# Kernel optimization log

Measured on AMD Instinct MI355X. Metric: run time of the kernel, lower is better.

Reference implementation:

```python
import jax, jax.numpy as jnp
import numpy as np

B, N, D, L = 4, 256, 512, 3  # batch, seq_len, input_dim, n_layer


def setup_inputs() -> dict:
    key = jax.random.key(0)
    ks = jax.random.split(key, 12)
    s = 0.02
    return {
        "x": jax.random.normal(ks[0], (B, N, D), dtype=jnp.float32),
        # Highway: L layers, each a gate Linear(D,D) and transform Linear(D,D)
        "hw_gate_w": jax.random.normal(ks[1], (L, D, D), dtype=jnp.float32) * s,
        "hw_gate_b": jnp.zeros((L, D), dtype=jnp.float32),
        "hw_tr_w": jax.random.normal(ks[2], (L, D, D), dtype=jnp.float32) * s,
        "hw_tr_b": jnp.zeros((L, D), dtype=jnp.float32),
        # link_weight MLP: Linear(2D,D) -> ReLU -> [Linear(D,D) -> ReLU]*(L-2) -> Linear(D,1) -> Sigmoid
        "lw0_w": jax.random.normal(ks[3], (D, 2 * D), dtype=jnp.float32) * s,
        "lw0_b": jnp.zeros((D,), dtype=jnp.float32),
        "lw1_w": jax.random.normal(ks[4], (D, D), dtype=jnp.float32) * s,
        "lw1_b": jnp.zeros((D,), dtype=jnp.float32),
        "lwo_w": jax.random.normal(ks[5], (1, D), dtype=jnp.float32) * s,
        "lwo_b": jnp.zeros((1,), dtype=jnp.float32),
    }


def _highway(x, gw, gb, tw, tb):
    # standard highway: y = g * relu(Wt x + bt) + (1 - g) * x, g = sigmoid(Wg x + bg)
    for i in range(gw.shape[0]):
        g = jax.nn.sigmoid(jnp.einsum('bnd,ed->bne', x, gw[i]) + gb[i])
        t = jax.nn.relu(jnp.einsum('bnd,ed->bne', x, tw[i]) + tb[i])
        x = g * t + (1.0 - g) * x
    return x


def reference(x, hw_gate_w, hw_gate_b, hw_tr_w, hw_tr_b,
              lw0_w, lw0_b, lw1_w, lw1_b, lwo_w, lwo_b):
    d = x.shape[-1]
    h = _highway(x, hw_gate_w, hw_gate_b, hw_tr_w, hw_tr_b)  # [B,N,D]
    # Fused pairwise-concat + first Linear: cat(h_i, h_j) @ W0.T ==
    # h_i @ W0[:, :D].T + h_j @ W0[:, D:].T  (avoids the [B,N*N,2D] tensor)
    a = jnp.einsum('bnd,ed->bne', h, lw0_w[:, :d])  # uses m1 (row i)
    b = jnp.einsum('bnd,ed->bne', h, lw0_w[:, d:])  # uses m2 (col j)
    z = jax.nn.relu(a[:, :, None, :] + b[:, None, :, :] + lw0_b)  # [B,N,N,D]
    # (dropout is identity in eval mode)
    z = jax.nn.relu(jnp.einsum('bijd,ed->bije', z, lw1_w) + lw1_b)  # n_layer-2 == 1 hidden layer
    out = jax.nn.sigmoid(jnp.einsum('bijd,d->bij', z, lwo_w[0]) + lwo_b[0])
    return out  # [B,N,N]
```

## Files before the change

### kernel.cpp

```cpp
#include <hip/hip_runtime.h>
#include <hip/hip_bf16.h>

#define BB 4
#define NN 256
#define DD 512

using short8   = __attribute__((ext_vector_type(8))) short;
using f32x4    = __attribute__((ext_vector_type(4))) float;
using uint32x4 = __attribute__((ext_vector_type(4))) unsigned int;

__device__ __forceinline__ unsigned short f2bf(float f) {
    unsigned int u = __float_as_uint(f);
    unsigned int r = (u + 0x7fffu + ((u >> 16) & 1u)) >> 16;
    return (unsigned short)r;
}

__device__ __forceinline__ unsigned cvtpk(float lo, float hi) {
    unsigned r;
    asm("v_cvt_pk_bf16_f32 %0, %1, %2" : "=v"(r) : "v"(lo), "v"(hi));
    return r;
}

template <int ROWS, int NW>
__device__ __forceinline__ void stage_rows(const unsigned short* src, int stride,
                                           short* dst, int tid) {
    int wave = tid >> 6, lane = tid & 63;
#pragma unroll
    for (int c = 0; c < ROWS / (8 * NW); ++c) {
        int rbase = (c * NW + wave) * 8;
        int row   = rbase + (lane >> 3);
        int slot  = (lane & 7) ^ (row & 7);
        const unsigned short* g = src + (size_t)row * stride + slot * 8;
        __builtin_amdgcn_global_load_lds(
            (const __attribute__((address_space(1))) void*)g,
            (__attribute__((address_space(3))) void*)(dst + rbase * 64),
            16, 0, 0);
    }
}

__device__ __forceinline__ short8 read_frag(const short* T, int rowBase, int k2) {
    int lane = threadIdx.x & 63;
    int row  = rowBase + (lane & 15);
    int slot = ((k2 * 4) + (lane >> 4)) ^ (row & 7);
    return *(const short8*)(T + row * 64 + slot * 8);
}

__global__ void prep_kernel(const float* __restrict__ x,
                            const float* __restrict__ gw, const float* __restrict__ tw,
                            const float* __restrict__ w0, const float* __restrict__ w1,
                            float* __restrict__ h0_f32, unsigned short* __restrict__ h0_bf,
                            unsigned short* __restrict__ wg_bf, unsigned short* __restrict__ wt_bf,
                            unsigned short* __restrict__ w0c_bf, unsigned short* __restrict__ w1_bf) {
    const int S_X = BB * NN * DD;
    const int S_W = 3 * DD * DD;
    const int S_W0 = 2 * DD * DD;
    int total = S_X + S_W + S_W + S_W0 + DD * DD;
    for (int idx = blockIdx.x * blockDim.x + threadIdx.x; idx < total;
         idx += gridDim.x * blockDim.x) {
        int t = idx;
        if (t < S_X) { float v = x[t]; h0_f32[t] = v; h0_bf[t] = f2bf(v); continue; }
        t -= S_X;
        if (t < S_W) { wg_bf[t] = f2bf(gw[t]); continue; }
        t -= S_W;
        if (t < S_W) { wt_bf[t] = f2bf(tw[t]); continue; }
        t -= S_W;
        if (t < S_W0) {
            int e = t >> 9, d = t & 511;
            float v = (e < DD) ? w0[e * (2 * DD) + d] : w0[(e - DD) * (2 * DD) + DD + d];
            w0c_bf[t] = f2bf(v); continue;
        }
        t -= S_W0;
        w1_bf[t] = f2bf(w1[t]);
    }
}

__global__ __launch_bounds__(256) void highway_kernel(
        const float* __restrict__ h_in, const unsigned short* __restrict__ hbf_in,
        const unsigned short* __restrict__ wg_bf, const unsigned short* __restrict__ wt_bf,
        const float* __restrict__ gb, const float* __restrict__ tb,
        float* __restrict__ h_out, unsigned short* __restrict__ hbf_out) {
    __shared__ short ht[64 * 64];
    __shared__ short wgt[64 * 64];
    __shared__ short wtt[64 * 64];
    int tid = threadIdx.x, lane = tid & 63, wave = tid >> 6;
    int mt = blockIdx.x >> 3, et = blockIdx.x & 7;
    int m0 = mt * 64, e0 = et * 64;
    int wm = wave >> 1, we = wave & 1;
    f32x4 gacc[2][2] = {}, tacc[2][2] = {};
    for (int ks = 0; ks < 8; ++ks) {
        int d0 = ks * 64;
        __syncthreads();
        stage_rows<64, 4>(hbf_in + (size_t)m0 * DD + d0, DD, ht, tid);
        stage_rows<64, 4>(wg_bf + (size_t)e0 * DD + d0, DD, wgt, tid);
        stage_rows<64, 4>(wt_bf + (size_t)e0 * DD + d0, DD, wtt, tid);
        __syncthreads();
#pragma unroll
        for (int k2 = 0; k2 < 2; ++k2) {
            short8 af[2], bg[2], bt[2];
#pragma unroll
            for (int f = 0; f < 2; ++f) af[f] = read_frag(ht, wm * 32 + f * 16, k2);
#pragma unroll
            for (int f = 0; f < 2; ++f) bg[f] = read_frag(wgt, we * 32 + f * 16, k2);
#pragma unroll
            for (int f = 0; f < 2; ++f) bt[f] = read_frag(wtt, we * 32 + f * 16, k2);
#pragma unroll
            for (int fm = 0; fm < 2; ++fm)
#pragma unroll
                for (int fn = 0; fn < 2; ++fn) {
                    gacc[fm][fn] = __builtin_amdgcn_mfma_f32_16x16x32_bf16(af[fm], bg[fn], gacc[fm][fn], 0, 0, 0);
                    tacc[fm][fn] = __builtin_amdgcn_mfma_f32_16x16x32_bf16(af[fm], bt[fn], tacc[fm][fn], 0, 0, 0);
                }
        }
    }
#pragma unroll
    for (int fm = 0; fm < 2; ++fm)
#pragma unroll
        for (int fn = 0; fn < 2; ++fn) {
            int e = e0 + we * 32 + fn * 16 + (lane & 15);
            float gbe = gb[e], tbe = tb[e];
#pragma unroll
            for (int r = 0; r < 4; ++r) {
                int m = m0 + wm * 32 + fm * 16 + (lane >> 4) * 4 + r;
                float g = 1.f / (1.f + __expf(-(gacc[fm][fn][r] + gbe)));
                float tv = tacc[fm][fn][r] + tbe; tv = tv > 0.f ? tv : 0.f;
                float ho = h_in[(size_t)m * DD + e];
                float hn = g * tv + (1.f - g) * ho;
                h_out[(size_t)m * DD + e] = hn;
                hbf_out[(size_t)m * DD + e] = f2bf(hn);
            }
        }
}

__global__ __launch_bounds__(256) void ab_kernel(
        const unsigned short* __restrict__ hbf, const unsigned short* __restrict__ w0c_bf,
        const float* __restrict__ lw0_b,
        float* __restrict__ a_out, float* __restrict__ b_out) {
    __shared__ short ht[64 * 64];
    __shared__ short wt_[128 * 64];
    int tid = threadIdx.x, lane = tid & 63, wave = tid >> 6;
    int mt = blockIdx.x >> 3, et = blockIdx.x & 7;
    int m0 = mt * 64, e0 = et * 128;
    int wm = wave >> 1, we = wave & 1;
    f32x4 acc[2][4] = {};
    for (int ks = 0; ks < 8; ++ks) {
        __syncthreads();
        stage_rows<64, 4>(hbf + (size_t)m0 * DD + ks * 64, DD, ht, tid);
        stage_rows<128, 4>(w0c_bf + (size_t)e0 * DD + ks * 64, DD, wt_, tid);
        __syncthreads();
#pragma unroll
        for (int k2 = 0; k2 < 2; ++k2) {
            short8 af[2], bf_[4];
#pragma unroll
            for (int f = 0; f < 2; ++f) af[f] = read_frag(ht, wm * 32 + f * 16, k2);
#pragma unroll
            for (int f = 0; f < 4; ++f) bf_[f] = read_frag(wt_, we * 64 + f * 16, k2);
#pragma unroll
            for (int fm = 0; fm < 2; ++fm)
#pragma unroll
                for (int fn = 0; fn < 4; ++fn)
                    acc[fm][fn] = __builtin_amdgcn_mfma_f32_16x16x32_bf16(af[fm], bf_[fn], acc[fm][fn], 0, 0, 0);
        }
    }
#pragma unroll
    for (int fm = 0; fm < 2; ++fm)
#pragma unroll
        for (int fn = 0; fn < 4; ++fn) {
            int e = e0 + we * 64 + fn * 16 + (lane & 15);
#pragma unroll
            for (int r = 0; r < 4; ++r) {
                int m = m0 + wm * 32 + fm * 16 + (lane >> 4) * 4 + r;
                float v = acc[fm][fn][r];
                if (e < DD) a_out[(size_t)m * DD + e] = v + lw0_b[e];
                else        b_out[(size_t)m * DD + (e - DD)] = v;
            }
        }
}


#define Z_LOADS(K)                                                            \
    {                                                                         \
        const int dl_ = (K) * 64 + s * 8;                                     \
        alo = *(const f32x4*)(arow + dl_);                                    \
        ahi = *(const f32x4*)(arow + dl_ + 4);                                \
        const float* b0_ = brow + (size_t)rr * DD + dl_;                      \
        const float* b1_ = brow + (size_t)(64 + rr) * DD + dl_;               \
        b0lo = *(const f32x4*)b0_; b0hi = *(const f32x4*)(b0_ + 4);           \
        b1lo = *(const f32x4*)b1_; b1hi = *(const f32x4*)(b1_ + 4);           \
    }

#define Z_MATH()                                                              \
    {                                                                         \
        zw0[0] = cvtpk(fmaxf(alo[0] + b0lo[0], 0.f), fmaxf(alo[1] + b0lo[1], 0.f)); \
        zw0[1] = cvtpk(fmaxf(alo[2] + b0lo[2], 0.f), fmaxf(alo[3] + b0lo[3], 0.f)); \
        zw0[2] = cvtpk(fmaxf(ahi[0] + b0hi[0], 0.f), fmaxf(ahi[1] + b0hi[1], 0.f)); \
        zw0[3] = cvtpk(fmaxf(ahi[2] + b0hi[2], 0.f), fmaxf(ahi[3] + b0hi[3], 0.f)); \
        zw1[0] = cvtpk(fmaxf(alo[0] + b1lo[0], 0.f), fmaxf(alo[1] + b1lo[1], 0.f)); \
        zw1[1] = cvtpk(fmaxf(alo[2] + b1lo[2], 0.f), fmaxf(alo[3] + b1lo[3], 0.f)); \
        zw1[2] = cvtpk(fmaxf(ahi[0] + b1hi[0], 0.f), fmaxf(ahi[1] + b1hi[1], 0.f)); \
        zw1[3] = cvtpk(fmaxf(ahi[2] + b1hi[2], 0.f), fmaxf(ahi[3] + b1hi[3], 0.f)); \
    }

#define Z_WRITE(BUF)                                                          \
    {                                                                         \
        *(uint32x4*)((BUF) + rr * 64 + ((s ^ (rr & 7)) * 8)) = zw0;           \
        const int r1_ = 64 + rr;                                              \
        *(uint32x4*)((BUF) + r1_ * 64 + ((s ^ (r1_ & 7)) * 8)) = zw1;         \
    }

__global__ __launch_bounds__(512, 2) void pair_kernel(
        const float* __restrict__ a_f32, const float* __restrict__ b_f32,
        const unsigned short* __restrict__ w1_bf,
        const float* __restrict__ lw1_b, const float* __restrict__ lwo_w,
        const float* __restrict__ lwo_b, float* __restrict__ out) {
    __shared__ short ws[2][512 * 64];
    __shared__ short zs[2][128 * 64];
    int tid = threadIdx.x, lane = tid & 63, wave = tid >> 6;
    int bid = blockIdx.x;
    int swz = (bid & 7) * 256 + (bid >> 3);
    int bb = swz >> 9, i = (swz >> 1) & 255, j0 = (swz & 1) * 128;
    const float* arow = a_f32 + (size_t)(bb * NN + i) * DD;
    const float* brow = b_f32 + (size_t)(bb * NN + j0) * DD;
    int s = tid & 7, rr = tid >> 3;
    int we = wave;

    f32x4 acc[8][4] = {};
    uint32x4 zw0, zw1;
    f32x4 alo, ahi, b0lo, b0hi, b1lo, b1hi;

    Z_LOADS(0)
    __builtin_amdgcn_sched_barrier(0);
    stage_rows<512, 8>(w1_bf, DD, ws[0], tid);
    __builtin_amdgcn_sched_barrier(0);
    Z_MATH()
    Z_WRITE(zs[0])
    asm volatile("s_waitcnt lgkmcnt(0)" ::: "memory");
    __builtin_amdgcn_s_barrier();
    asm volatile("s_waitcnt vmcnt(0)" ::: "memory");
    __builtin_amdgcn_s_barrier();

#pragma unroll
    for (int k = 0; k < 8; ++k) {
        const short* zc = zs[k & 1];
        const short* wc = ws[k & 1];

        if (k < 7) {
            Z_LOADS(k + 1)
            __builtin_amdgcn_sched_barrier(0);
            stage_rows<512, 8>(w1_bf + (size_t)(k + 1) * 64, DD,
                               ws[(k + 1) & 1], tid);
            __builtin_amdgcn_sched_barrier(0);
        }

#pragma unroll
        for (int k2 = 0; k2 < 2; ++k2) {
            short8 bfr[4];
#pragma unroll
            for (int f = 0; f < 4; ++f) bfr[f] = read_frag(wc, we * 64 + f * 16, k2);
#pragma unroll
            for (int fh = 0; fh < 2; ++fh) {
                short8 af[4];
#pragma unroll
                for (int f = 0; f < 4; ++f) af[f] = read_frag(zc, (fh * 4 + f) * 16, k2);
                __builtin_amdgcn_s_setprio(1);
#pragma unroll
                for (int fm = 0; fm < 4; ++fm)
#pragma unroll
                    for (int fn = 0; fn < 4; ++fn)
                        acc[fh * 4 + fm][fn] = __builtin_amdgcn_mfma_f32_16x16x32_bf16(
                            af[fm], bfr[fn], acc[fh * 4 + fm][fn], 0, 0, 0);
                __builtin_amdgcn_s_setprio(0);
            }
        }

        if (k < 7) {
            Z_MATH()
            Z_WRITE(zs[(k + 1) & 1])
            asm volatile("s_waitcnt lgkmcnt(0)" ::: "memory");
        }
        __builtin_amdgcn_s_barrier();
        if (k < 7) {
            asm volatile("s_waitcnt vmcnt(0)" ::: "memory");
            __builtin_amdgcn_s_barrier();
        }
    }

    __syncthreads();
    float* s_red = (float*)zs;
#pragma unroll
    for (int fm = 0; fm < 8; ++fm) {
        float red[4] = {0.f, 0.f, 0.f, 0.f};
#pragma unroll
        for (int fn = 0; fn < 4; ++fn) {
            int e = we * 64 + fn * 16 + (lane & 15);
            float b1e = lw1_b[e], woe = lwo_w[e];
#pragma unroll
            for (int r = 0; r < 4; ++r) {
                float v = acc[fm][fn][r] + b1e;
                red[r] += (v > 0.f) ? v * woe : 0.f;
            }
        }
#pragma unroll
        for (int mask = 1; mask < 16; mask <<= 1)
#pragma unroll
            for (int r = 0; r < 4; ++r) red[r] += __shfl_xor(red[r], mask, 64);
        if ((lane & 15) == 0) {
#pragma unroll
            for (int r = 0; r < 4; ++r)
                s_red[we * 128 + fm * 16 + (lane >> 4) * 4 + r] = red[r];
        }
    }
    __syncthreads();
    if (tid < 128) {
        float v = lwo_b[0];
#pragma unroll
        for (int w8 = 0; w8 < 8; ++w8) v += s_red[w8 * 128 + tid];
        out[((size_t)(bb * NN + i)) * NN + j0 + tid] = 1.f / (1.f + __expf(-v));
    }
}

extern "C" void kernel_launch(void* const* d_in, const int* in_sizes, int n_in,
                              void* d_out, int out_size, void* d_ws, size_t ws_size,
                              hipStream_t stream) {
    const float* x    = (const float*)d_in[0];
    const float* gw   = (const float*)d_in[1];
    const float* gb   = (const float*)d_in[2];
    const float* tw   = (const float*)d_in[3];
    const float* tb   = (const float*)d_in[4];
    const float* w0   = (const float*)d_in[5];
    const float* w0b  = (const float*)d_in[6];
    const float* w1   = (const float*)d_in[7];
    const float* w1b_ = (const float*)d_in[8];
    const float* wo   = (const float*)d_in[9];
    const float* wob  = (const float*)d_in[10];
    float* out = (float*)d_out;

    char* w = (char*)d_ws;
    float* hA  = (float*)w;            w += (size_t)BB * NN * DD * 4;
    float* hB  = (float*)w;            w += (size_t)BB * NN * DD * 4;
    unsigned short* hbA = (unsigned short*)w; w += (size_t)BB * NN * DD * 2;
    unsigned short* hbB = (unsigned short*)w; w += (size_t)BB * NN * DD * 2;
    float* a_f = (float*)w;            w += (size_t)BB * NN * DD * 4;
    float* b_f = (float*)w;            w += (size_t)BB * NN * DD * 4;
    unsigned short* wg_bf  = (unsigned short*)w; w += (size_t)3 * DD * DD * 2;
    unsigned short* wt_bf  = (unsigned short*)w; w += (size_t)3 * DD * DD * 2;
    unsigned short* w0c_bf = (unsigned short*)w; w += (size_t)2 * DD * DD * 2;
    unsigned short* w1_bf  = (unsigned short*)w; w += (size_t)DD * DD * 2;

    prep_kernel<<<1024, 256, 0, stream>>>(x, gw, tw, w0, w1, hA, hbA, wg_bf, wt_bf, w0c_bf, w1_bf);

    highway_kernel<<<128, 256, 0, stream>>>(hA, hbA, wg_bf + 0 * DD * DD, wt_bf + 0 * DD * DD,
                                            gb + 0 * DD, tb + 0 * DD, hB, hbB);
    highway_kernel<<<128, 256, 0, stream>>>(hB, hbB, wg_bf + 1 * DD * DD, wt_bf + 1 * DD * DD,
                                            gb + 1 * DD, tb + 1 * DD, hA, hbA);
    highway_kernel<<<128, 256, 0, stream>>>(hA, hbA, wg_bf + 2 * DD * DD, wt_bf + 2 * DD * DD,
                                            gb + 2 * DD, tb + 2 * DD, hB, hbB);

    ab_kernel<<<128, 256, 0, stream>>>(hbB, w0c_bf, w0b, a_f, b_f);

    pair_kernel<<<2048, 512, 0, stream>>>(a_f, b_f, w1_bf, w1b_, wo, wob, out);
}
```

Measured before the change: 223.9 us.

## Split pair kernel across output-feature quarters and add a combine kernel

```diff
diff --git a/kernel.cpp b/kernel.cpp
--- a/kernel.cpp
+++ b/kernel.cpp
@@ -207,29 +207,32 @@
         *(uint32x4*)((BUF) + r1_ * 64 + ((s ^ (r1_ & 7)) * 8)) = zw1;         \
     }
 
-__global__ __launch_bounds__(512, 2) void pair_kernel(
+__global__ __launch_bounds__(512, 4) void pair_kernel(
         const float* __restrict__ a_f32, const float* __restrict__ b_f32,
         const unsigned short* __restrict__ w1_bf,
         const float* __restrict__ lw1_b, const float* __restrict__ lwo_w,
-        const float* __restrict__ lwo_b, float* __restrict__ out) {
-    __shared__ short ws[2][512 * 64];
+        float* __restrict__ part) {
+    __shared__ short ws[2][128 * 64];
     __shared__ short zs[2][128 * 64];
     int tid = threadIdx.x, lane = tid & 63, wave = tid >> 6;
     int bid = blockIdx.x;
-    int swz = (bid & 7) * 256 + (bid >> 3);
+    int eq = bid >> 11;
+    int ij = bid & 2047;
+    int swz = (ij & 7) * 256 + (ij >> 3);
     int bb = swz >> 9, i = (swz >> 1) & 255, j0 = (swz & 1) * 128;
+    int e0 = eq * 128;
     const float* arow = a_f32 + (size_t)(bb * NN + i) * DD;
     const float* brow = b_f32 + (size_t)(bb * NN + j0) * DD;
     int s = tid & 7, rr = tid >> 3;
-    int we = wave;
-
-    f32x4 acc[8][4] = {};
+    int jg = wave >> 1, eg = wave & 1;
+
+    f32x4 acc[2][4] = {};
     uint32x4 zw0, zw1;
     f32x4 alo, ahi, b0lo, b0hi, b1lo, b1hi;
 
     Z_LOADS(0)
     __builtin_amdgcn_sched_barrier(0);
-    stage_rows<512, 8>(w1_bf, DD, ws[0], tid);
+    stage_rows<128, 8>(w1_bf + (size_t)e0 * DD, DD, ws[0], tid);
     __builtin_amdgcn_sched_barrier(0);
     Z_MATH()
     Z_WRITE(zs[0])
@@ -246,30 +249,26 @@
         if (k < 7) {
             Z_LOADS(k + 1)
             __builtin_amdgcn_sched_barrier(0);
-            stage_rows<512, 8>(w1_bf + (size_t)(k + 1) * 64, DD,
+            stage_rows<128, 8>(w1_bf + (size_t)e0 * DD + (k + 1) * 64, DD,
                                ws[(k + 1) & 1], tid);
             __builtin_amdgcn_sched_barrier(0);
         }
 
 #pragma unroll
         for (int k2 = 0; k2 < 2; ++k2) {
-            short8 bfr[4];
-#pragma unroll
-            for (int f = 0; f < 4; ++f) bfr[f] = read_frag(wc, we * 64 + f * 16, k2);
-#pragma unroll
-            for (int fh = 0; fh < 2; ++fh) {
-                short8 af[4];
-#pragma unroll
-                for (int f = 0; f < 4; ++f) af[f] = read_frag(zc, (fh * 4 + f) * 16, k2);
-                __builtin_amdgcn_s_setprio(1);
-#pragma unroll
-                for (int fm = 0; fm < 4; ++fm)
-#pragma unroll
-                    for (int fn = 0; fn < 4; ++fn)
-                        acc[fh * 4 + fm][fn] = __builtin_amdgcn_mfma_f32_16x16x32_bf16(
-                            af[fm], bfr[fn], acc[fh * 4 + fm][fn], 0, 0, 0);
-                __builtin_amdgcn_s_setprio(0);
-            }
+            short8 af[2], bfr[4];
+#pragma unroll
+            for (int f = 0; f < 4; ++f) bfr[f] = read_frag(wc, eg * 64 + f * 16, k2);
+#pragma unroll
+            for (int f = 0; f < 2; ++f) af[f] = read_frag(zc, jg * 32 + f * 16, k2);
+            __builtin_amdgcn_s_setprio(1);
+#pragma unroll
+            for (int fm = 0; fm < 2; ++fm)
+#pragma unroll
+                for (int fn = 0; fn < 4; ++fn)
+                    acc[fm][fn] = __builtin_amdgcn_mfma_f32_16x16x32_bf16(
+                        af[fm], bfr[fn], acc[fm][fn], 0, 0, 0);
+            __builtin_amdgcn_s_setprio(0);
         }
 
         if (k < 7) {
@@ -287,11 +286,11 @@
     __syncthreads();
     float* s_red = (float*)zs;
 #pragma unroll
-    for (int fm = 0; fm < 8; ++fm) {
+    for (int fm = 0; fm < 2; ++fm) {
         float red[4] = {0.f, 0.f, 0.f, 0.f};
 #pragma unroll
         for (int fn = 0; fn < 4; ++fn) {
-            int e = we * 64 + fn * 16 + (lane & 15);
+            int e = e0 + eg * 64 + fn * 16 + (lane & 15);
             float b1e = lw1_b[e], woe = lwo_w[e];
 #pragma unroll
             for (int r = 0; r < 4; ++r) {
@@ -306,15 +305,25 @@
         if ((lane & 15) == 0) {
 #pragma unroll
             for (int r = 0; r < 4; ++r)
-                s_red[we * 128 + fm * 16 + (lane >> 4) * 4 + r] = red[r];
+                s_red[eg * 128 + jg * 32 + fm * 16 + (lane >> 4) * 4 + r] = red[r];
         }
     }
     __syncthreads();
     if (tid < 128) {
-        float v = lwo_b[0];
-#pragma unroll
-        for (int w8 = 0; w8 < 8; ++w8) v += s_red[w8 * 128 + tid];
-        out[((size_t)(bb * NN + i)) * NN + j0 + tid] = 1.f / (1.f + __expf(-v));
+        float v = s_red[tid] + s_red[128 + tid];
+        part[(size_t)eq * (BB * NN * NN) + ((size_t)(bb * NN + i)) * NN + j0 + tid] = v;
+    }
+}
+
+__global__ __launch_bounds__(256) void combine_kernel(
+        const float* __restrict__ part, const float* __restrict__ lwo_b,
+        float* __restrict__ out) {
+    const int T = BB * NN * NN;
+    int idx = blockIdx.x * 256 + threadIdx.x;
+    if (idx < T) {
+        float v = part[idx] + part[T + idx] + part[2 * T + idx] +
+                  part[3 * T + idx] + lwo_b[0];
+        out[idx] = 1.f / (1.f + __expf(-v));
     }
 }
 
@@ -346,6 +355,8 @@
     unsigned short* w0c_bf = (unsigned short*)w; w += (size_t)2 * DD * DD * 2;
     unsigned short* w1_bf  = (unsigned short*)w; w += (size_t)DD * DD * 2;
 
+    float* part = hA;
+
     prep_kernel<<<1024, 256, 0, stream>>>(x, gw, tw, w0, w1, hA, hbA, wg_bf, wt_bf, w0c_bf, w1_bf);
 
     highway_kernel<<<128, 256, 0, stream>>>(hA, hbA, wg_bf + 0 * DD * DD, wt_bf + 0 * DD * DD,
@@ -357,5 +368,7 @@
 
     ab_kernel<<<128, 256, 0, stream>>>(hbB, w0c_bf, w0b, a_f, b_f);
 
-    pair_kernel<<<2048, 512, 0, stream>>>(a_f, b_f, w1_bf, w1b_, wo, wob, out);
-}
+    pair_kernel<<<8192, 512, 0, stream>>>(a_f, b_f, w1_bf, w1b_, wo, part);
+
+    combine_kernel<<<(BB * NN * NN + 255) / 256, 256, 0, stream>>>(part, wob, out);
+}
```

Result: slower. 247.3 us (+10.5%).

## Halve K-tile to 32 and triple-buffer W1 staging with one barrier per step

Applied to the files above, without the earlier changes.

```diff
diff --git a/kernel.cpp b/kernel.cpp
--- a/kernel.cpp
+++ b/kernel.cpp
@@ -43,6 +43,30 @@
     int row  = rowBase + (lane & 15);
     int slot = ((k2 * 4) + (lane >> 4)) ^ (row & 7);
     return *(const short8*)(T + row * 64 + slot * 8);
+}
+
+template <int ROWS, int NW>
+__device__ __forceinline__ void stage_rows32(const unsigned short* src, int stride,
+                                             short* dst, int tid) {
+    int wave = tid >> 6, lane = tid & 63;
+#pragma unroll
+    for (int c = 0; c < ROWS / (16 * NW); ++c) {
+        int rbase = (c * NW + wave) * 16;
+        int row   = rbase + (lane >> 2);
+        int slot  = (lane & 3) ^ ((row >> 1) & 3);
+        const unsigned short* g = src + (size_t)row * stride + slot * 8;
+        __builtin_amdgcn_global_load_lds(
+            (const __attribute__((address_space(1))) void*)g,
+            (__attribute__((address_space(3))) void*)(dst + rbase * 32),
+            16, 0, 0);
+    }
+}
+
+__device__ __forceinline__ short8 read_frag32(const short* T, int rowBase) {
+    int lane = threadIdx.x & 63;
+    int row  = rowBase + (lane & 15);
+    int slot = (lane >> 4) ^ ((row >> 1) & 3);
+    return *(const short8*)(T + row * 32 + slot * 8);
 }
 
 __global__ void prep_kernel(const float* __restrict__ x,
@@ -177,34 +201,24 @@
 }
 
 
-#define Z_LOADS(K)                                                            \
+#define AB_LOADS(K)                                                           \
     {                                                                         \
-        const int dl_ = (K) * 64 + s * 8;                                     \
+        const int dl_ = (K) * 32 + s4 * 8;                                    \
         alo = *(const f32x4*)(arow + dl_);                                    \
         ahi = *(const f32x4*)(arow + dl_ + 4);                                \
-        const float* b0_ = brow + (size_t)rr * DD + dl_;                      \
-        const float* b1_ = brow + (size_t)(64 + rr) * DD + dl_;               \
-        b0lo = *(const f32x4*)b0_; b0hi = *(const f32x4*)(b0_ + 4);           \
-        b1lo = *(const f32x4*)b1_; b1hi = *(const f32x4*)(b1_ + 4);           \
-    }
-
-#define Z_MATH()                                                              \
+        const float* bp_ = brow + (size_t)rr * DD + dl_;                      \
+        blo = *(const f32x4*)bp_;                                             \
+        bhi = *(const f32x4*)(bp_ + 4);                                       \
+    }
+
+#define Z_MATH_WRITE(BUF)                                                     \
     {                                                                         \
-        zw0[0] = cvtpk(fmaxf(alo[0] + b0lo[0], 0.f), fmaxf(alo[1] + b0lo[1], 0.f)); \
-        zw0[1] = cvtpk(fmaxf(alo[2] + b0lo[2], 0.f), fmaxf(alo[3] + b0lo[3], 0.f)); \
-        zw0[2] = cvtpk(fmaxf(ahi[0] + b0hi[0], 0.f), fmaxf(ahi[1] + b0hi[1], 0.f)); \
-        zw0[3] = cvtpk(fmaxf(ahi[2] + b0hi[2], 0.f), fmaxf(ahi[3] + b0hi[3], 0.f)); \
-        zw1[0] = cvtpk(fmaxf(alo[0] + b1lo[0], 0.f), fmaxf(alo[1] + b1lo[1], 0.f)); \
-        zw1[1] = cvtpk(fmaxf(alo[2] + b1lo[2], 0.f), fmaxf(alo[3] + b1lo[3], 0.f)); \
-        zw1[2] = cvtpk(fmaxf(ahi[0] + b1hi[0], 0.f), fmaxf(ahi[1] + b1hi[1], 0.f)); \
-        zw1[3] = cvtpk(fmaxf(ahi[2] + b1hi[2], 0.f), fmaxf(ahi[3] + b1hi[3], 0.f)); \
-    }
-
-#define Z_WRITE(BUF)                                                          \
-    {                                                                         \
-        *(uint32x4*)((BUF) + rr * 64 + ((s ^ (rr & 7)) * 8)) = zw0;           \
-        const int r1_ = 64 + rr;                                              \
-        *(uint32x4*)((BUF) + r1_ * 64 + ((s ^ (r1_ & 7)) * 8)) = zw1;         \
+        uint32x4 zw;                                                          \
+        zw[0] = cvtpk(fmaxf(alo[0] + blo[0], 0.f), fmaxf(alo[1] + blo[1], 0.f)); \
+        zw[1] = cvtpk(fmaxf(alo[2] + blo[2], 0.f), fmaxf(alo[3] + blo[3], 0.f)); \
+        zw[2] = cvtpk(fmaxf(ahi[0] + bhi[0], 0.f), fmaxf(ahi[1] + bhi[1], 0.f)); \
+        zw[3] = cvtpk(fmaxf(ahi[2] + bhi[2], 0.f), fmaxf(ahi[3] + bhi[3], 0.f)); \
+        *(uint32x4*)((BUF) + rr * 32 + ((s4 ^ ((rr >> 1) & 3)) * 8)) = zw;    \
     }
 
 __global__ __launch_bounds__(512, 2) void pair_kernel(
@@ -212,74 +226,68 @@
         const unsigned short* __restrict__ w1_bf,
         const float* __restrict__ lw1_b, const float* __restrict__ lwo_w,
         const float* __restrict__ lwo_b, float* __restrict__ out) {
-    __shared__ short ws[2][512 * 64];
-    __shared__ short zs[2][128 * 64];
+    __shared__ short ws[3][512 * 32];
+    __shared__ short zs[2][128 * 32];
     int tid = threadIdx.x, lane = tid & 63, wave = tid >> 6;
     int bid = blockIdx.x;
     int swz = (bid & 7) * 256 + (bid >> 3);
     int bb = swz >> 9, i = (swz >> 1) & 255, j0 = (swz & 1) * 128;
     const float* arow = a_f32 + (size_t)(bb * NN + i) * DD;
     const float* brow = b_f32 + (size_t)(bb * NN + j0) * DD;
-    int s = tid & 7, rr = tid >> 3;
+    int s4 = tid & 3, rr = tid >> 2;
     int we = wave;
 
     f32x4 acc[8][4] = {};
-    uint32x4 zw0, zw1;
-    f32x4 alo, ahi, b0lo, b0hi, b1lo, b1hi;
-
-    Z_LOADS(0)
+    f32x4 alo, ahi, blo, bhi;
+
+    AB_LOADS(0)
     __builtin_amdgcn_sched_barrier(0);
-    stage_rows<512, 8>(w1_bf, DD, ws[0], tid);
+    stage_rows32<512, 8>(w1_bf, DD, ws[0], tid);
     __builtin_amdgcn_sched_barrier(0);
-    Z_MATH()
-    Z_WRITE(zs[0])
+    Z_MATH_WRITE(zs[0])
     asm volatile("s_waitcnt lgkmcnt(0)" ::: "memory");
+    stage_rows32<512, 8>(w1_bf + 32, DD, ws[1], tid);
+    __builtin_amdgcn_sched_barrier(0);
+    asm volatile("s_waitcnt vmcnt(4)" ::: "memory");
     __builtin_amdgcn_s_barrier();
-    asm volatile("s_waitcnt vmcnt(0)" ::: "memory");
-    __builtin_amdgcn_s_barrier();
-
-#pragma unroll
-    for (int k = 0; k < 8; ++k) {
+
+#pragma unroll
+    for (int k = 0; k < 16; ++k) {
         const short* zc = zs[k & 1];
-        const short* wc = ws[k & 1];
-
-        if (k < 7) {
-            Z_LOADS(k + 1)
+        const short* wc = ws[k % 3];
+
+        if (k < 15) {
+            AB_LOADS(k + 1)
             __builtin_amdgcn_sched_barrier(0);
-            stage_rows<512, 8>(w1_bf + (size_t)(k + 1) * 64, DD,
-                               ws[(k + 1) & 1], tid);
+            if (k < 14)
+                stage_rows32<512, 8>(w1_bf + (size_t)(k + 2) * 32, DD,
+                                     ws[(k + 2) % 3], tid);
             __builtin_amdgcn_sched_barrier(0);
         }
 
-#pragma unroll
-        for (int k2 = 0; k2 < 2; ++k2) {
-            short8 bfr[4];
-#pragma unroll
-            for (int f = 0; f < 4; ++f) bfr[f] = read_frag(wc, we * 64 + f * 16, k2);
-#pragma unroll
-            for (int fh = 0; fh < 2; ++fh) {
-                short8 af[4];
-#pragma unroll
-                for (int f = 0; f < 4; ++f) af[f] = read_frag(zc, (fh * 4 + f) * 16, k2);
-                __builtin_amdgcn_s_setprio(1);
-#pragma unroll
-                for (int fm = 0; fm < 4; ++fm)
-#pragma unroll
-                    for (int fn = 0; fn < 4; ++fn)
-                        acc[fh * 4 + fm][fn] = __builtin_amdgcn_mfma_f32_16x16x32_bf16(
-                            af[fm], bfr[fn], acc[fh * 4 + fm][fn], 0, 0, 0);
-                __builtin_amdgcn_s_setprio(0);
-            }
-        }
-
-        if (k < 7) {
-            Z_MATH()
-            Z_WRITE(zs[(k + 1) & 1])
+        {
+            short8 bfr[4], af[8];
+#pragma unroll
+            for (int f = 0; f < 4; ++f) bfr[f] = read_frag32(wc, we * 64 + f * 16);
+#pragma unroll
+            for (int f = 0; f < 8; ++f) af[f] = read_frag32(zc, f * 16);
             asm volatile("s_waitcnt lgkmcnt(0)" ::: "memory");
-        }
-        __builtin_amdgcn_s_barrier();
-        if (k < 7) {
-            asm volatile("s_waitcnt vmcnt(0)" ::: "memory");
+            __builtin_amdgcn_sched_barrier(0);
+            __builtin_amdgcn_s_setprio(1);
+#pragma unroll
+            for (int fm = 0; fm < 8; ++fm)
+#pragma unroll
+                for (int fn = 0; fn < 4; ++fn)
+                    acc[fm][fn] = __builtin_amdgcn_mfma_f32_16x16x32_bf16(
+                        af[fm], bfr[fn], acc[fm][fn], 0, 0, 0);
+            __builtin_amdgcn_s_setprio(0);
+        }
+
+        if (k < 15) {
+            Z_MATH_WRITE(zs[(k + 1) & 1])
+            asm volatile("s_waitcnt lgkmcnt(0)" ::: "memory");
+            if (k < 14) asm volatile("s_waitcnt vmcnt(4)" ::: "memory");
+            else        asm volatile("s_waitcnt vmcnt(0)" ::: "memory");
             __builtin_amdgcn_s_barrier();
         }
     }
```

Result: no change. 224.2 us (+0.1%).
